# Optimization experiments

Hardware: AMD Instinct MI355X
Metric: run time of the kernel (lower is better)

The kernel has to match this reference:

```python
import jax, jax.numpy as jnp
import numpy as np

D = 1024
H = 16
HD = D // H
SCALE = HD ** -0.5


def setup_inputs() -> dict:
    key = jax.random.key(0)
    ks = jax.random.split(key, 5)
    x = jax.random.normal(ks[0], (2, 2048, D), dtype=jnp.float32)
    s = 1.0 / np.sqrt(D)
    W_qkv = jax.random.uniform(ks[1], (D, 3 * D), jnp.float32, -s, s)
    b_qkv = jax.random.uniform(ks[2], (3 * D,), jnp.float32, -s, s)
    W_out = jax.random.uniform(ks[3], (D, D), jnp.float32, -s, s)
    b_out = jax.random.uniform(ks[4], (D,), jnp.float32, -s, s)
    return {"x": x, "W_qkv": W_qkv, "b_qkv": b_qkv, "W_out": W_out, "b_out": b_out}


def reference(x, W_qkv, b_qkv, W_out, b_out):
    B, S, _ = x.shape
    qkv = x @ W_qkv + b_qkv                       # [B,S,3D]
    qkv = qkv.reshape(B, S, 3, H, HD)
    q, k, v = jnp.moveaxis(qkv, 2, 0)             # each [B,S,H,HD]
    # scores: [B,H,S,S]
    scores = jnp.einsum("bshd,bthd->bhst", q, k) * SCALE
    attn = jax.nn.softmax(scores, axis=-1)        # dropout is identity in eval mode
    out = jnp.einsum("bhst,bthd->bshd", attn, v)  # [B,S,H,HD]
    out = out.reshape(B, S, H * HD)
    return out @ W_out + b_out
```

## Files before the change

kernel.cpp:

```cpp
#include <hip/hip_runtime.h>

typedef unsigned short u16;
typedef unsigned int   u32;

using short8 = __attribute__((ext_vector_type(8))) short;
using f32x4  = __attribute__((ext_vector_type(4))) float;
using half4  = __attribute__((ext_vector_type(4))) _Float16;

#define QSCALE 0.18033688011112042f

__device__ __forceinline__ u16 f2bf(float f) {
  u32 u = __float_as_uint(f);
  return (u16)((u + 0x8000u) >> 16);
}
__device__ __forceinline__ u16 f2h(float f) {
  _Float16 h = (_Float16)f;
  return __builtin_bit_cast(u16, h);
}

__device__ __forceinline__ void gld16(const u16* g, u16* l) {
  __builtin_amdgcn_global_load_lds(
      (const __attribute__((address_space(1))) unsigned int*)g,
      (__attribute__((address_space(3))) unsigned int*)l, 16, 0, 0);
}

__global__ __launch_bounds__(256) void cvt_x(const float* __restrict__ in,
                                             u16* __restrict__ out) {
  int idx = blockIdx.x * 256 + threadIdx.x;
  float4 v = reinterpret_cast<const float4*>(in)[idx];
  ushort4 o;
  o.x = f2bf(v.x); o.y = f2bf(v.y); o.z = f2bf(v.z); o.w = f2bf(v.w);
  reinterpret_cast<ushort4*>(out)[idx] = o;
}

__global__ __launch_bounds__(256) void transpose_w(const float* __restrict__ in,
                                                   u16* __restrict__ out,
                                                   int R, int C) {
  __shared__ u32 s[32][33];
  int c0 = blockIdx.x * 32, r0 = blockIdx.y * 32;
  int j = threadIdx.x & 31, i0 = threadIdx.x >> 5;
#pragma unroll
  for (int p = 0; p < 4; ++p) {
    int i = i0 + p * 8;
    s[i][j] = f2bf(in[(size_t)(r0 + i) * C + c0 + j]);
  }
  __syncthreads();
#pragma unroll
  for (int p = 0; p < 4; ++p) {
    int jj = i0 + p * 8;
    out[(size_t)(c0 + jj) * R + r0 + j] = (u16)s[j][jj];
  }
}

template <int EPI, int MT>
__global__ __launch_bounds__(256, 3) void gemm_bt(
    const u16* __restrict__ A, const u16* __restrict__ Bt,
    const float* __restrict__ bias, float* __restrict__ c_out,
    u16* __restrict__ q_out, u16* __restrict__ k_out, u16* __restrict__ vt_out,
    int M, int N, int K) {
  __shared__ __align__(16) u16 As[32 * MT * 32];
  __shared__ __align__(16) u16 Bs[128 * 32];
  const int tid = threadIdx.x;
  const int lane = tid & 63;
  const int wv = tid >> 6;
  const int l16 = lane & 15, quad = lane >> 4;
  const int wm = wv & 1, wn = wv >> 1;
  const int bx = blockIdx.x, by = blockIdx.y;

  const u16* Ab = A + (size_t)by * (32 * MT) * K;
  const u16* Bb = Bt + (size_t)bx * 128 * K;

  const f32x4 fzero = {0.0f, 0.0f, 0.0f, 0.0f};
  f32x4 acc[MT][4];
#pragma unroll
  for (int i = 0; i < MT; ++i)
#pragma unroll
    for (int j = 0; j < 4; ++j) acc[i][j] = fzero;

  for (int k0 = 0; k0 < K; k0 += 32) {
    __syncthreads();
#pragma unroll
    for (int p = 0; p < MT / 2; ++p) {
      int id = p * 256 + tid;
      int row = id >> 2, blk = id & 3;
      int gc = k0 + ((blk ^ (row & 3)) << 3);
      gld16(Ab + (size_t)row * K + gc, &As[id << 3]);
    }
#pragma unroll
    for (int p = 0; p < 2; ++p) {
      int id = p * 256 + tid;
      int row = id >> 2, blk = id & 3;
      int gc = k0 + ((blk ^ (row & 3)) << 3);
      gld16(Bb + (size_t)row * K + gc, &Bs[id << 3]);
    }
    __syncthreads();
    short8 af[MT], bfr[4];
#pragma unroll
    for (int mi = 0; mi < MT; ++mi) {
      int row = wm * (MT * 16) + mi * 16 + l16;
      af[mi] = *reinterpret_cast<const short8*>(&As[row * 32 + ((quad ^ (row & 3)) << 3)]);
    }
#pragma unroll
    for (int ni = 0; ni < 4; ++ni) {
      int row = wn * 64 + ni * 16 + l16;
      bfr[ni] = *reinterpret_cast<const short8*>(&Bs[row * 32 + ((quad ^ (row & 3)) << 3)]);
    }
#pragma unroll
    for (int mi = 0; mi < MT; ++mi)
#pragma unroll
      for (int ni = 0; ni < 4; ++ni)
        acc[mi][ni] = __builtin_amdgcn_mfma_f32_16x16x32_bf16(af[mi], bfr[ni], acc[mi][ni], 0, 0, 0);
  }

#pragma unroll
  for (int mi = 0; mi < MT; ++mi)
#pragma unroll
    for (int ni = 0; ni < 4; ++ni) {
      int col = bx * 128 + wn * 64 + ni * 16 + l16;
      float bv = bias[col];
      int row0 = by * (32 * MT) + wm * (MT * 16) + mi * 16 + quad * 4;
      if (EPI == 1) {
#pragma unroll
        for (int r = 0; r < 4; ++r)
          c_out[(size_t)(row0 + r) * N + col] = acc[mi][ni][r] + bv;
      } else {
        int which = col >> 10, rem = col & 1023;
        int h = rem >> 6, d = rem & 63;
        int b = row0 >> 11, sq0 = row0 & 2047;
        int bh = (b << 4) + h;
        if (which == 2) {
          int tile = sq0 >> 6;
          int sub = ((sq0 >> 2) & 15) ^ (d & 15);
          ushort4 pk;
          pk.x = f2h(acc[mi][ni][0] + bv);
          pk.y = f2h(acc[mi][ni][1] + bv);
          pk.z = f2h(acc[mi][ni][2] + bv);
          pk.w = f2h(acc[mi][ni][3] + bv);
          *reinterpret_cast<ushort4*>(
              &vt_out[(size_t)bh * 131072 + tile * 4096 + d * 64 + (sub << 2)]) = pk;
        } else {
          size_t base = (size_t)(bh * 2048 + sq0) * 64 + d;
#pragma unroll
          for (int r = 0; r < 4; ++r) {
            float val = acc[mi][ni][r] + bv;
            if (which == 0) q_out[base + r * 64] = f2bf(val * QSCALE);
            else            k_out[base + r * 64] = f2bf(val);
          }
        }
      }
    }
}

__global__ __launch_bounds__(256, 3) void attn(
    const u16* __restrict__ q_buf, const u16* __restrict__ k_buf,
    const u16* __restrict__ vt_buf, u16* __restrict__ o_buf) {
  __shared__ __align__(16) u16 smem[2][2][4096];
  __shared__ __align__(16) float lred[256];

  const int tid = threadIdx.x;
  const int lane = tid & 63, w = tid >> 6;
  const int l16 = lane & 15, quad = lane >> 4;
  const int bh = blockIdx.y, q0 = blockIdx.x * 64;

  const u16* qg = q_buf + (size_t)bh * 131072 + q0 * 64;
  const u16* kg = k_buf + (size_t)bh * 131072;
  const u16* vg = vt_buf + (size_t)bh * 131072;

  short8 qb[4][2];
#pragma unroll
  for (int qi = 0; qi < 4; ++qi)
#pragma unroll
    for (int kk = 0; kk < 2; ++kk)
      qb[qi][kk] = *reinterpret_cast<const short8*>(
          qg + (qi * 16 + l16) * 64 + kk * 32 + quad * 8);

#pragma unroll
  for (int p = 0; p < 2; ++p) {
    int id = p * 256 + tid;
    int row = id >> 3, blk = id & 7;
    gld16(kg + row * 64 + ((blk ^ (row & 7)) << 3), &smem[0][0][id << 3]);
    gld16(vg + id * 8, &smem[0][1][id << 3]);
  }

  const f32x4 fzero = {0.0f, 0.0f, 0.0f, 0.0f};
  f32x4 o_acc[4][4];
  float l_acc[4] = {0.f, 0.f, 0.f, 0.f};
#pragma unroll
  for (int qi = 0; qi < 4; ++qi)
#pragma unroll
    for (int nd = 0; nd < 4; ++nd) o_acc[qi][nd] = fzero;

  const int kr = w * 16 + l16;
  const int ka_off0 = kr * 64 + (((0 * 4 + quad) ^ (kr & 7)) << 3);
  const int ka_off1 = kr * 64 + (((1 * 4 + quad) ^ (kr & 7)) << 3);
  const int vb_off = l16 * 64 + ((((w * 4 + quad) ^ l16)) << 2);

  __syncthreads();

  for (int i = 0; i < 32; ++i) {
    const int buf = i & 1;
    if (i + 1 < 32) {
      const int nxt = buf ^ 1;
#pragma unroll
      for (int p = 0; p < 2; ++p) {
        int id = p * 256 + tid;
        int row = id >> 3, blk = id & 7;
        gld16(kg + ((i + 1) * 64 + row) * 64 + ((blk ^ (row & 7)) << 3),
              &smem[nxt][0][id << 3]);
        gld16(vg + (i + 1) * 4096 + id * 8, &smem[nxt][1][id << 3]);
      }
    }

    f32x4 s[4];
#pragma unroll
    for (int qi = 0; qi < 4; ++qi) s[qi] = fzero;
    {
      short8 ka0 = *reinterpret_cast<const short8*>(&smem[buf][0][ka_off0]);
      short8 ka1 = *reinterpret_cast<const short8*>(&smem[buf][0][ka_off1]);
#pragma unroll
      for (int qi = 0; qi < 4; ++qi) {
        s[qi] = __builtin_amdgcn_mfma_f32_16x16x32_bf16(ka0, qb[qi][0], s[qi], 0, 0, 0);
        s[qi] = __builtin_amdgcn_mfma_f32_16x16x32_bf16(ka1, qb[qi][1], s[qi], 0, 0, 0);
      }
    }

    half4 pa[4];
#pragma unroll
    for (int qi = 0; qi < 4; ++qi) {
      float p0 = __builtin_amdgcn_exp2f(s[qi][0]);
      float p1 = __builtin_amdgcn_exp2f(s[qi][1]);
      float p2 = __builtin_amdgcn_exp2f(s[qi][2]);
      float p3 = __builtin_amdgcn_exp2f(s[qi][3]);
      l_acc[qi] += (p0 + p1) + (p2 + p3);
      pa[qi][0] = (_Float16)p0; pa[qi][1] = (_Float16)p1;
      pa[qi][2] = (_Float16)p2; pa[qi][3] = (_Float16)p3;
    }

#pragma unroll
    for (int nd = 0; nd < 4; ++nd) {
      half4 vb = *reinterpret_cast<const half4*>(&smem[buf][1][vb_off + nd * 1024]);
#pragma unroll
      for (int qi = 0; qi < 4; ++qi)
        o_acc[qi][nd] = __builtin_amdgcn_mfma_f32_16x16x16f16(pa[qi], vb, o_acc[qi][nd], 0, 0, 0);
    }

    __syncthreads();
  }

#pragma unroll
  for (int qi = 0; qi < 4; ++qi) {
    l_acc[qi] += __shfl_xor(l_acc[qi], 16, 64);
    l_acc[qi] += __shfl_xor(l_acc[qi], 32, 64);
  }
  if (lane < 16) {
#pragma unroll
    for (int qi = 0; qi < 4; ++qi) lred[(w * 4 + qi) * 16 + lane] = l_acc[qi];
  }

  float* fb = (float*)smem;
  const int b = bh >> 4, h = bh & 15;

#pragma unroll
  for (int phase = 0; phase < 2; ++phase) {
#pragma unroll
    for (int qq = 0; qq < 2; ++qq) {
      int qi = phase * 2 + qq;
#pragma unroll
      for (int nd = 0; nd < 4; ++nd)
        *reinterpret_cast<f32x4*>(&fb[((w * 2 + qq) * 4 + nd) * 256 + lane * 4]) =
            o_acc[qi][nd];
    }
    __syncthreads();
    if ((w >> 1) == phase) {
      const int sel = w & 1;
      f32x4 lv = fzero;
#pragma unroll
      for (int wp = 0; wp < 4; ++wp)
        lv += *reinterpret_cast<const f32x4*>(&lred[(wp * 4 + w) * 16 + quad * 4]);
      f32x4 os[4];
#pragma unroll
      for (int nd = 0; nd < 4; ++nd) {
        os[nd] = fzero;
#pragma unroll
        for (int wp = 0; wp < 4; ++wp)
          os[nd] += *reinterpret_cast<const f32x4*>(
              &fb[((wp * 2 + sel) * 4 + nd) * 256 + lane * 4]);
      }
#pragma unroll
      for (int r = 0; r < 4; ++r) {
        int sq = q0 + w * 16 + quad * 4 + r;
        float inv = 1.0f / lv[r];
        size_t base = (size_t)(b * 2048 + sq) * 1024 + h * 64;
#pragma unroll
        for (int nd = 0; nd < 4; ++nd)
          o_buf[base + nd * 16 + l16] = f2bf(os[nd][r] * inv);
      }
    }
    __syncthreads();
  }
}

extern "C" void kernel_launch(void* const* d_in, const int* in_sizes, int n_in,
                              void* d_out, int out_size, void* d_ws, size_t ws_size,
                              hipStream_t stream) {
  (void)in_sizes; (void)n_in; (void)out_size; (void)ws_size;
  const float* x     = (const float*)d_in[0];
  const float* W_qkv = (const float*)d_in[1];
  const float* b_qkv = (const float*)d_in[2];
  const float* W_out = (const float*)d_in[3];
  const float* b_out = (const float*)d_in[4];
  float* out = (float*)d_out;

  char* ws = (char*)d_ws;
  u16* x_bf   = (u16*)(ws);
  u16* wqkv_t = (u16*)(ws + 8388608);
  u16* wout_t = (u16*)(ws + 14680064);
  u16* q_buf  = (u16*)(ws + 16777216);
  u16* k_buf  = (u16*)(ws + 25165824);
  u16* vt_buf = (u16*)(ws + 33554432);
  u16* o_bf   = (u16*)(ws + 41943040);

  cvt_x<<<4096, 256, 0, stream>>>(x, x_bf);
  transpose_w<<<dim3(96, 32), 256, 0, stream>>>(W_qkv, wqkv_t, 1024, 3072);
  transpose_w<<<dim3(32, 32), 256, 0, stream>>>(W_out, wout_t, 1024, 1024);
  gemm_bt<0, 4><<<dim3(24, 32), 256, 0, stream>>>(x_bf, wqkv_t, b_qkv, nullptr,
                                                  q_buf, k_buf, vt_buf, 4096, 3072, 1024);
  attn<<<dim3(32, 32), 256, 0, stream>>>(q_buf, k_buf, vt_buf, o_bf);
  gemm_bt<1, 2><<<dim3(8, 64), 256, 0, stream>>>(o_bf, wout_t, b_out, out,
                                                 nullptr, nullptr, nullptr, 4096, 1024, 1024);
}
```

Measured before the change: 198.4 us.

## Halve attention query tile to 32 rows and double grid for more occupancy

Each attention block now handles 32 query rows instead of 64, doubling the grid to 64x32 blocks and raising launch bounds to 5 blocks per CU. Register use per thread drops (fewer Q fragments and accumulators), which allows more waves per CU. The cross-wave reduction epilogue is rewritten to store the row sums in the shared buffer and have each wave write one 16-column slice. In exchange, every K/V tile is now loaded from global memory twice as often per query row, and there is more MFMA-free overhead per tile.

```diff
diff --git a/kernel.cpp b/kernel.cpp
--- a/kernel.cpp
+++ b/kernel.cpp
@@ -151,24 +151,23 @@
     }
 }
 
-__global__ __launch_bounds__(256, 3) void attn(
+__global__ __launch_bounds__(256, 5) void attn(
     const u16* __restrict__ q_buf, const u16* __restrict__ k_buf,
     const u16* __restrict__ vt_buf, u16* __restrict__ o_buf) {
   __shared__ __align__(16) u16 smem[2][2][4096];
-  __shared__ __align__(16) float lred[256];
 
   const int tid = threadIdx.x;
   const int lane = tid & 63, w = tid >> 6;
   const int l16 = lane & 15, quad = lane >> 4;
-  const int bh = blockIdx.y, q0 = blockIdx.x * 64;
+  const int bh = blockIdx.y, q0 = blockIdx.x * 32;
 
   const u16* qg = q_buf + (size_t)bh * 131072 + q0 * 64;
   const u16* kg = k_buf + (size_t)bh * 131072;
   const u16* vg = vt_buf + (size_t)bh * 131072;
 
-  short8 qb[4][2];
-#pragma unroll
-  for (int qi = 0; qi < 4; ++qi)
+  short8 qb[2][2];
+#pragma unroll
+  for (int qi = 0; qi < 2; ++qi)
 #pragma unroll
     for (int kk = 0; kk < 2; ++kk)
       qb[qi][kk] = *reinterpret_cast<const short8*>(
@@ -183,17 +182,17 @@
   }
 
   const f32x4 fzero = {0.0f, 0.0f, 0.0f, 0.0f};
-  f32x4 o_acc[4][4];
-  float l_acc[4] = {0.f, 0.f, 0.f, 0.f};
-#pragma unroll
-  for (int qi = 0; qi < 4; ++qi)
+  f32x4 o_acc[2][4];
+  float l_acc[2] = {0.f, 0.f};
+#pragma unroll
+  for (int qi = 0; qi < 2; ++qi)
 #pragma unroll
     for (int nd = 0; nd < 4; ++nd) o_acc[qi][nd] = fzero;
 
   const int kr = w * 16 + l16;
-  const int ka_off0 = kr * 64 + (((0 * 4 + quad) ^ (kr & 7)) << 3);
-  const int ka_off1 = kr * 64 + (((1 * 4 + quad) ^ (kr & 7)) << 3);
-  const int vb_off = l16 * 64 + ((((w * 4 + quad) ^ l16)) << 2);
+  const int ka_off0 = kr * 64 + ((quad ^ (kr & 7)) << 3);
+  const int ka_off1 = kr * 64 + (((4 + quad) ^ (kr & 7)) << 3);
+  const int vb_off = l16 * 64 + (((w * 4 + quad) ^ l16) << 2);
 
   __syncthreads();
 
@@ -211,22 +210,18 @@
       }
     }
 
-    f32x4 s[4];
-#pragma unroll
-    for (int qi = 0; qi < 4; ++qi) s[qi] = fzero;
-    {
-      short8 ka0 = *reinterpret_cast<const short8*>(&smem[buf][0][ka_off0]);
-      short8 ka1 = *reinterpret_cast<const short8*>(&smem[buf][0][ka_off1]);
-#pragma unroll
-      for (int qi = 0; qi < 4; ++qi) {
-        s[qi] = __builtin_amdgcn_mfma_f32_16x16x32_bf16(ka0, qb[qi][0], s[qi], 0, 0, 0);
-        s[qi] = __builtin_amdgcn_mfma_f32_16x16x32_bf16(ka1, qb[qi][1], s[qi], 0, 0, 0);
-      }
-    }
-
-    half4 pa[4];
-#pragma unroll
-    for (int qi = 0; qi < 4; ++qi) {
+    short8 ka0 = *reinterpret_cast<const short8*>(&smem[buf][0][ka_off0]);
+    short8 ka1 = *reinterpret_cast<const short8*>(&smem[buf][0][ka_off1]);
+    f32x4 s[2];
+#pragma unroll
+    for (int qi = 0; qi < 2; ++qi) {
+      s[qi] = __builtin_amdgcn_mfma_f32_16x16x32_bf16(ka0, qb[qi][0], fzero, 0, 0, 0);
+      s[qi] = __builtin_amdgcn_mfma_f32_16x16x32_bf16(ka1, qb[qi][1], s[qi], 0, 0, 0);
+    }
+
+    half4 pa[2];
+#pragma unroll
+    for (int qi = 0; qi < 2; ++qi) {
       float p0 = __builtin_amdgcn_exp2f(s[qi][0]);
       float p1 = __builtin_amdgcn_exp2f(s[qi][1]);
       float p2 = __builtin_amdgcn_exp2f(s[qi][2]);
@@ -240,7 +235,7 @@
     for (int nd = 0; nd < 4; ++nd) {
       half4 vb = *reinterpret_cast<const half4*>(&smem[buf][1][vb_off + nd * 1024]);
 #pragma unroll
-      for (int qi = 0; qi < 4; ++qi)
+      for (int qi = 0; qi < 2; ++qi)
         o_acc[qi][nd] = __builtin_amdgcn_mfma_f32_16x16x16f16(pa[qi], vb, o_acc[qi][nd], 0, 0, 0);
     }
 
@@ -248,53 +243,31 @@
   }
 
 #pragma unroll
-  for (int qi = 0; qi < 4; ++qi) {
+  for (int qi = 0; qi < 2; ++qi) {
     l_acc[qi] += __shfl_xor(l_acc[qi], 16, 64);
     l_acc[qi] += __shfl_xor(l_acc[qi], 32, 64);
   }
-  if (lane < 16) {
-#pragma unroll
-    for (int qi = 0; qi < 4; ++qi) lred[(w * 4 + qi) * 16 + lane] = l_acc[qi];
-  }
 
   float* fb = (float*)smem;
   const int b = bh >> 4, h = bh & 15;
-
-#pragma unroll
-  for (int phase = 0; phase < 2; ++phase) {
-#pragma unroll
-    for (int qq = 0; qq < 2; ++qq) {
-      int qi = phase * 2 + qq;
-#pragma unroll
-      for (int nd = 0; nd < 4; ++nd)
-        *reinterpret_cast<f32x4*>(&fb[((w * 2 + qq) * 4 + nd) * 256 + lane * 4]) =
-            o_acc[qi][nd];
-    }
-    __syncthreads();
-    if ((w >> 1) == phase) {
-      const int sel = w & 1;
-      f32x4 lv = fzero;
-#pragma unroll
-      for (int wp = 0; wp < 4; ++wp)
-        lv += *reinterpret_cast<const f32x4*>(&lred[(wp * 4 + w) * 16 + quad * 4]);
-      f32x4 os[4];
-#pragma unroll
-      for (int nd = 0; nd < 4; ++nd) {
-        os[nd] = fzero;
-#pragma unroll
-        for (int wp = 0; wp < 4; ++wp)
-          os[nd] += *reinterpret_cast<const f32x4*>(
-              &fb[((wp * 2 + sel) * 4 + nd) * 256 + lane * 4]);
-      }
-#pragma unroll
-      for (int r = 0; r < 4; ++r) {
-        int sq = q0 + w * 16 + quad * 4 + r;
-        float inv = 1.0f / lv[r];
-        size_t base = (size_t)(b * 2048 + sq) * 1024 + h * 64;
-#pragma unroll
-        for (int nd = 0; nd < 4; ++nd)
-          o_buf[base + nd * 16 + l16] = f2bf(os[nd][r] * inv);
-      }
+#pragma unroll
+  for (int qi = 0; qi < 2; ++qi) {
+#pragma unroll
+    for (int nd = 0; nd < 4; ++nd)
+      *reinterpret_cast<f32x4*>(&fb[((w * 4 + nd) * 64 + lane) * 4]) = o_acc[qi][nd];
+    if (lane < 16) fb[4096 + w * 16 + lane] = l_acc[qi];
+    __syncthreads();
+    f32x4 os = fzero, lv = fzero;
+#pragma unroll
+    for (int wp = 0; wp < 4; ++wp) {
+      os += *reinterpret_cast<const f32x4*>(&fb[((wp * 4 + w) * 64 + lane) * 4]);
+      lv += *reinterpret_cast<const f32x4*>(&fb[4096 + wp * 16 + quad * 4]);
+    }
+#pragma unroll
+    for (int r = 0; r < 4; ++r) {
+      int sq = q0 + qi * 16 + quad * 4 + r;
+      o_buf[(size_t)(b * 2048 + sq) * 1024 + h * 64 + w * 16 + l16] =
+          f2bf(os[r] / lv[r]);
     }
     __syncthreads();
   }
@@ -325,7 +298,7 @@
   transpose_w<<<dim3(32, 32), 256, 0, stream>>>(W_out, wout_t, 1024, 1024);
   gemm_bt<0, 4><<<dim3(24, 32), 256, 0, stream>>>(x_bf, wqkv_t, b_qkv, nullptr,
                                                   q_buf, k_buf, vt_buf, 4096, 3072, 1024);
-  attn<<<dim3(32, 32), 256, 0, stream>>>(q_buf, k_buf, vt_buf, o_bf);
+  attn<<<dim3(64, 32), 256, 0, stream>>>(q_buf, k_buf, vt_buf, o_bf);
   gemm_bt<1, 2><<<dim3(8, 64), 256, 0, stream>>>(o_bf, wout_t, b_out, out,
                                                  nullptr, nullptr, nullptr, 4096, 1024, 1024);
 }
```

After: 196.8 us. No clear change (-0.8%).
